# Optimization experiments

Hardware: AMD Instinct MI355X
Metric: run time of the kernel (lower is better)

## Reference

```python
import jax, jax.numpy as jnp
import numpy as np

L, D, H, DH, S, B, V = 8, 1024, 16, 64, 1024, 4, 32000
EPS = 1e-5


def layernorm(x, s, b):
    m = x.mean(-1, keepdims=True)
    v = ((x - m) ** 2).mean(-1, keepdims=True)
    return (x - m) * jax.lax.rsqrt(v + EPS) * s + b


def setup_inputs() -> dict:
    key = jax.random.key(0)
    ks = jax.random.split(key, 12)
    sd = 0.02
    inp = {
        'idx': jax.random.randint(ks[0], (B, S), 0, V),
        'tok_emb': jax.random.normal(ks[1], (V, D), jnp.float32) * sd,
        'pos_emb': jax.random.normal(ks[2], (S, D), jnp.float32) * sd,
        'ln1_s': jnp.ones((L, D), jnp.float32),
        'ln1_b': jnp.zeros((L, D), jnp.float32),
        'wq': jax.random.normal(ks[3], (L, H, D, DH), jnp.float32) * sd,
        'wk': jax.random.normal(ks[4], (L, H, D, DH), jnp.float32) * sd,
        'wv': jax.random.normal(ks[5], (L, H, D, DH), jnp.float32) * sd,
        'wproj': jax.random.normal(ks[6], (L, D, D), jnp.float32) * sd,  # stored [D_in, D_out]
        'ln2_s': jnp.ones((L, D), jnp.float32),
        'ln2_b': jnp.zeros((L, D), jnp.float32),
        'w1': jax.random.normal(ks[7], (L, D, 4 * D), jnp.float32) * sd,
        'b1': jnp.zeros((L, 4 * D), jnp.float32),
        'w2': jax.random.normal(ks[8], (L, 4 * D, D), jnp.float32) * sd,
        'b2': jnp.zeros((L, D), jnp.float32),
        'lnf_s': jnp.ones((D,), jnp.float32),
        'lnf_b': jnp.zeros((D,), jnp.float32),
        'lm_w': jax.random.normal(ks[9], (D, V), jnp.float32) * sd,  # stored [D_in, V]
        'lm_b': jnp.zeros((V,), jnp.float32),
    }
    return inp


def reference(idx, tok_emb, pos_emb, ln1_s, ln1_b, wq, wk, wv, wproj,
              ln2_s, ln2_b, w1, b1, w2, b2, lnf_s, lnf_b, lm_w, lm_b):
    T = idx.shape[1]
    x = tok_emb[idx] + pos_emb[:T]  # [B,T,D]
    mask = jnp.tril(jnp.ones((T, T), bool))
    scale = DH ** -0.5
    for l in range(L):  # fixed small layer count
        h = layernorm(x, ln1_s[l], ln1_b[l])
        q = jnp.einsum('bsd,hde->bhse', h, wq[l])
        k = jnp.einsum('bsd,hde->bhse', h, wk[l])
        v = jnp.einsum('bsd,hde->bhse', h, wv[l])
        att = jnp.einsum('bhse,bhte->bhst', q, k) * scale
        att = jnp.where(mask, att, -jnp.inf)
        att = jax.nn.softmax(att, axis=-1)  # dropout=0.0 -> identity
        o = jnp.einsum('bhst,bhte->bhse', att, v)
        o = o.transpose(0, 2, 1, 3).reshape(x.shape)  # concat heads: [B,T,H*DH]
        x = x + o @ wproj[l]
        h2 = layernorm(x, ln2_s[l], ln2_b[l])
        x = x + jax.nn.relu(h2 @ w1[l] + b1[l]) @ w2[l] + b2[l]
    x = layernorm(x, lnf_s, lnf_b)
    logits = x @ lm_w + lm_b  # [B,T,V]
    return logits
```

## Files before the change

### kernel.cpp

```cpp
#include <hip/hip_runtime.h>
#include <hip/hip_bf16.h>

#define LL 8
#define DD 1024
#define HH 16
#define DHH 64
#define SS 1024
#define BB 4
#define VV 32000
#define MM (BB * SS)

typedef unsigned short u16;
typedef __attribute__((ext_vector_type(8))) short short8v;
typedef __attribute__((ext_vector_type(4))) float f32x4;
typedef unsigned int __attribute__((address_space(1))) guint;
typedef unsigned int __attribute__((address_space(3))) luint;

__device__ __forceinline__ float bf2f_lo(unsigned u) { return __uint_as_float(u << 16); }
__device__ __forceinline__ u16 f2bf(float f) {
  unsigned x = __float_as_uint(f);
  return (u16)((x + 0x7fffu + ((x >> 16) & 1u)) >> 16);
}

__global__ __launch_bounds__(256) void embed_kernel(
    const int* __restrict__ idx, const float* __restrict__ tok,
    const float* __restrict__ pos, float* __restrict__ x) {
  int i = blockIdx.x * blockDim.x + threadIdx.x;
  int elem = i * 4;
  int row = elem / DD;
  int d = elem % DD;
  int s = row % SS;
  int t = idx[row];
  float4 tv = *(const float4*)(tok + (size_t)t * DD + d);
  float4 pv = *(const float4*)(pos + (size_t)s * DD + d);
  tv.x += pv.x; tv.y += pv.y; tv.z += pv.z; tv.w += pv.w;
  *(float4*)(x + (size_t)elem) = tv;
}

__global__ __launch_bounds__(256) void ln_bf16_kernel(
    const float* __restrict__ x, const float* __restrict__ sc,
    const float* __restrict__ bi, u16* __restrict__ out) {
  const int row = blockIdx.x;
  const int tid = threadIdx.x;
  __shared__ float red[4];
  float4 v = ((const float4*)(x + (size_t)row * DD))[tid];
  float s = v.x + v.y + v.z + v.w;
  #pragma unroll
  for (int off = 32; off; off >>= 1) s += __shfl_down(s, off);
  if ((tid & 63) == 0) red[tid >> 6] = s;
  __syncthreads();
  float mean = (red[0] + red[1] + red[2] + red[3]) * (1.f / DD);
  float dx = v.x - mean, dy = v.y - mean, dz = v.z - mean, dw = v.w - mean;
  float vs = dx * dx + dy * dy + dz * dz + dw * dw;
  __syncthreads();
  #pragma unroll
  for (int off = 32; off; off >>= 1) vs += __shfl_down(vs, off);
  if ((tid & 63) == 0) red[tid >> 6] = vs;
  __syncthreads();
  float var = (red[0] + red[1] + red[2] + red[3]) * (1.f / DD);
  float rstd = rsqrtf(var + 1e-5f);
  float4 s4 = ((const float4*)sc)[tid];
  float4 b4 = ((const float4*)bi)[tid];
  ushort4 o;
  o.x = f2bf(dx * rstd * s4.x + b4.x);
  o.y = f2bf(dy * rstd * s4.y + b4.y);
  o.z = f2bf(dz * rstd * s4.z + b4.z);
  o.w = f2bf(dw * rstd * s4.w + b4.w);
  *(ushort4*)(out + (size_t)row * DD + tid * 4) = o;
}

template <bool HEADW>
__global__ __launch_bounds__(256) void convT_kernel(
    const float* __restrict__ W, u16* __restrict__ BT, int K, int N,
    size_t lstride) {
  __shared__ float tile[32][33];
  const int n0 = blockIdx.x * 32, k0 = blockIdx.y * 32, l = blockIdx.z;
  const int tx = threadIdx.x & 31, ty = threadIdx.x >> 5;
  const float* Wl;
  int ld;
  if (HEADW) {
    const int h = n0 >> 6;
    Wl = W + ((size_t)(l * HH + h) * K) * 64 + (n0 & 63);
    ld = 64;
  } else {
    Wl = W + (size_t)l * K * N + n0;
    ld = N;
  }
  #pragma unroll
  for (int i = 0; i < 4; ++i)
    tile[ty + 8 * i][tx] = Wl[(size_t)(k0 + ty + 8 * i) * ld + tx];
  __syncthreads();
  u16* out = BT + (size_t)l * lstride;
  #pragma unroll
  for (int i = 0; i < 4; ++i)
    out[(size_t)(n0 + ty + 8 * i) * K + k0 + tx] = f2bf(tile[tx][ty + 8 * i]);
}

template <bool BIAS, bool RELU, bool RESID, bool OBF16>
__global__ __launch_bounds__(256) void gemm_mfma(
    const u16* __restrict__ A, const u16* __restrict__ BT,
    const float* __restrict__ bias, const float* __restrict__ resid,
    void* __restrict__ Cv, int M, int N, int K) {
  __shared__ u16 As[128 * 64];
  __shared__ u16 Bs[128 * 64];
  const int tid = threadIdx.x;
  const int lane = tid & 63, wave = tid >> 6;
  const int m0 = blockIdx.x * 128, n0 = blockIdx.y * 128;
  const int wr = (wave >> 1) * 64, wc = (wave & 1) * 64;
  const int srow = tid >> 3;
  const int scol = (((tid & 7) ^ (srow & 7)) * 8);
  const u16* Ag = A + (size_t)(m0 + srow) * K + scol;
  const u16* Bg = BT + (size_t)(n0 + srow) * K + scol;

  f32x4 acc[4][4] = {};
  for (int k0 = 0; k0 < K; k0 += 64) {
    #pragma unroll
    for (int c = 0; c < 4; ++c) {
      __builtin_amdgcn_global_load_lds(
          (const guint*)(Ag + k0 + (size_t)c * 32 * K),
          (luint*)(As + c * 2048 + tid * 8), 16, 0, 0);
      __builtin_amdgcn_global_load_lds(
          (const guint*)(Bg + k0 + (size_t)c * 32 * K),
          (luint*)(Bs + c * 2048 + tid * 8), 16, 0, 0);
    }
    __syncthreads();
    #pragma unroll
    for (int kk = 0; kk < 64; kk += 32) {
      const int chA = (((kk >> 3) | (lane >> 4)) ^ (lane & 7)) * 8;
      short8v av[4], bv[4];
      #pragma unroll
      for (int i = 0; i < 4; ++i)
        av[i] = *(const short8v*)(As + (wr + i * 16 + (lane & 15)) * 64 + chA);
      #pragma unroll
      for (int j = 0; j < 4; ++j)
        bv[j] = *(const short8v*)(Bs + (wc + j * 16 + (lane & 15)) * 64 + chA);
      #pragma unroll
      for (int i = 0; i < 4; ++i)
        #pragma unroll
        for (int j = 0; j < 4; ++j)
          acc[i][j] = __builtin_amdgcn_mfma_f32_16x16x32_bf16(av[i], bv[j], acc[i][j], 0, 0, 0);
    }
    __syncthreads();
  }
  #pragma unroll
  for (int i = 0; i < 4; ++i) {
    #pragma unroll
    for (int j = 0; j < 4; ++j) {
      const int col = n0 + wc + j * 16 + (lane & 15);
      #pragma unroll
      for (int r = 0; r < 4; ++r) {
        const int row = m0 + wr + i * 16 + (lane >> 4) * 4 + r;
        float v = acc[i][j][r];
        if (BIAS) v += bias[col];
        if (RELU) v = fmaxf(v, 0.f);
        if (RESID) v += resid[(size_t)row * N + col];
        if (OBF16)
          ((u16*)Cv)[(size_t)row * N + col] = f2bf(v);
        else
          ((float*)Cv)[(size_t)row * N + col] = v;
      }
    }
  }
}

#define LDA_(BUF, KH, F) \
  (*(const short8v*)&As[BUF][KH][(wm * 128 + (F) * 16 + (lane & 15)) * 32 + rg])
#define LDB_(BUF, KH, NF) \
  (*(const short8v*)&Bs[BUF][KH][(wn * 64 + (NF) * 16 + (lane & 15)) * 32 + rg])
#define PH_A(BUF, KH, FB) { a0 = LDA_(BUF, KH, (FB) + 0); a1 = LDA_(BUF, KH, (FB) + 1); \
                            a2 = LDA_(BUF, KH, (FB) + 2); a3 = LDA_(BUF, KH, (FB) + 3); }
#define PH_B(BUF, KH)     { b0 = LDB_(BUF, KH, 0); b1 = LDB_(BUF, KH, 1); \
                            b2 = LDB_(BUF, KH, 2); b3 = LDB_(BUF, KH, 3); }
#define STAGE_A(BUF, KH, KT) do { \
  __builtin_amdgcn_global_load_lds((const guint*)(Abase + (KT) * 64 + (KH) * 32), \
      (luint*)(&As[BUF][KH][tid * 8]), 16, 0, 0); \
  __builtin_amdgcn_global_load_lds((const guint*)(Abase + (size_t)128 * K + (KT) * 64 + (KH) * 32), \
      (luint*)(&As[BUF][KH][(tid + 512) * 8]), 16, 0, 0); \
} while (0)
#define STAGE_B(BUF, KH, KT) do { \
  __builtin_amdgcn_global_load_lds((const guint*)(Bbase + (KT) * 64 + (KH) * 32), \
      (luint*)(&Bs[BUF][KH][tid * 8]), 16, 0, 0); \
  __builtin_amdgcn_global_load_lds((const guint*)(Bbase + (size_t)128 * K + (KT) * 64 + (KH) * 32), \
      (luint*)(&Bs[BUF][KH][(tid + 512) * 8]), 16, 0, 0); \
} while (0)
#define MFMA_ROW(F, AQ) \
  acc[F][0] = __builtin_amdgcn_mfma_f32_16x16x32_bf16(AQ, b0, acc[F][0], 0, 0, 0); \
  acc[F][1] = __builtin_amdgcn_mfma_f32_16x16x32_bf16(AQ, b1, acc[F][1], 0, 0, 0); \
  acc[F][2] = __builtin_amdgcn_mfma_f32_16x16x32_bf16(AQ, b2, acc[F][2], 0, 0, 0); \
  acc[F][3] = __builtin_amdgcn_mfma_f32_16x16x32_bf16(AQ, b3, acc[F][3], 0, 0, 0);
#define MFMA16(FB) MFMA_ROW((FB) + 0, a0) MFMA_ROW((FB) + 1, a1) \
                   MFMA_ROW((FB) + 2, a2) MFMA_ROW((FB) + 3, a3)
#define BARRIER __builtin_amdgcn_s_barrier()
#define LGKM0 asm volatile("s_waitcnt lgkmcnt(0)" ::: "memory")
#define MEMFENCE asm volatile("" ::: "memory")

#define TILE8(CUR, KT, ST1, ST2, V1STR, DOV3, V3STR) { \
  const int cur_ = (CUR); \
  MEMFENCE; \
  PH_B(cur_, 0); PH_A(cur_, 0, 0); \
  if (ST1) { STAGE_A(cur_ ^ 1, 1, (KT) + 1); } \
  BARRIER; LGKM0; \
  __builtin_amdgcn_s_setprio(1); MFMA16(0); __builtin_amdgcn_s_setprio(0); \
  BARRIER; MEMFENCE; \
  PH_A(cur_, 0, 4); \
  if (ST1) { STAGE_B(cur_ ^ 1, 1, (KT) + 1); } \
  asm volatile("s_waitcnt " V1STR ::: "memory"); \
  BARRIER; LGKM0; \
  __builtin_amdgcn_s_setprio(1); MFMA16(4); __builtin_amdgcn_s_setprio(0); \
  BARRIER; MEMFENCE; \
  PH_B(cur_, 1); PH_A(cur_, 1, 0); \
  if (ST2) { STAGE_A(cur_, 0, (KT) + 2); } \
  BARRIER; LGKM0; \
  __builtin_amdgcn_s_setprio(1); MFMA16(0); __builtin_amdgcn_s_setprio(0); \
  BARRIER; MEMFENCE; \
  PH_A(cur_, 1, 4); \
  if (ST2) { STAGE_B(cur_, 0, (KT) + 2); } \
  if (DOV3) { asm volatile("s_waitcnt " V3STR ::: "memory"); } \
  BARRIER; LGKM0; \
  __builtin_amdgcn_s_setprio(1); MFMA16(4); __builtin_amdgcn_s_setprio(0); \
  BARRIER; \
}

template <bool BIAS, bool RELU, bool RESID, bool OBF16>
__global__ __launch_bounds__(512, 2) void gemm8(
    const u16* __restrict__ A, const u16* __restrict__ BT,
    const float* __restrict__ bias, const float* __restrict__ resid,
    void* __restrict__ Cv, int M, int N, int K) {
  __shared__ u16 As[2][2][8192];
  __shared__ u16 Bs[2][2][8192];
  const int tid = threadIdx.x;
  const int lane = tid & 63, wave = tid >> 6;
  const int wm = wave >> 2, wn = wave & 3;
  const int nwg = gridDim.x;
  const int bid = blockIdx.x;
  const int wg = ((nwg & 7) == 0) ? ((bid & 7) * (nwg >> 3) + (bid >> 3)) : bid;
  const int nmt = M >> 8;
  const int m0 = (wg % nmt) * 256;
  const int n0 = (wg / nmt) * 256;
  const int NT = K >> 6;
  const int sr = tid >> 2;
  const int ssc = (((tid & 3) ^ ((tid >> 3) & 3)) * 8);
  const u16* Abase = A + (size_t)(m0 + sr) * K + ssc;
  const u16* Bbase = BT + (size_t)(n0 + sr) * K + ssc;
  const int rg = (((lane >> 4) ^ ((lane >> 1) & 3)) * 8);

  f32x4 acc[8][4] = {};
  short8v a0, a1, a2, a3, b0, b1, b2, b3;

  STAGE_A(0, 0, 0); STAGE_B(0, 0, 0);
  STAGE_A(0, 1, 0); STAGE_B(0, 1, 0);
  STAGE_A(1, 0, 1); STAGE_B(1, 0, 1);
  asm volatile("s_waitcnt vmcnt(8)" ::: "memory");
  BARRIER;

  int kt = 0;
  for (; kt < NT - 2; ++kt) {
    TILE8(kt & 1, kt, true, true, "vmcnt(8)", true, "vmcnt(8)");
  }
  TILE8(kt & 1, kt, true, false, "vmcnt(8)", true, "vmcnt(4)");
  ++kt;
  TILE8(kt & 1, kt, false, false, "vmcnt(0)", false, "vmcnt(0)");

  #pragma unroll
  for (int f = 0; f < 8; ++f) {
    #pragma unroll
    for (int n = 0; n < 4; ++n) {
      const int col = n0 + wn * 64 + n * 16 + (lane & 15);
      #pragma unroll
      for (int r = 0; r < 4; ++r) {
        const int row = m0 + wm * 128 + f * 16 + (lane >> 4) * 4 + r;
        float v = acc[f][n][r];
        if (BIAS) v += bias[col];
        if (RELU) v = fmaxf(v, 0.f);
        if (RESID) v += resid[(size_t)row * N + col];
        if (OBF16)
          ((u16*)Cv)[(size_t)row * N + col] = f2bf(v);
        else
          ((float*)Cv)[(size_t)row * N + col] = v;
      }
    }
  }
}

__global__ __launch_bounds__(256) void gemm_fb(
    const u16* __restrict__ A, const float* __restrict__ B,
    const float* __restrict__ bias, float* __restrict__ C, int M, int N, int K) {
  __shared__ alignas(16) float Asm[16][68];
  __shared__ alignas(16) float Bsm[16][68];
  const int tid = threadIdx.x;
  const int tx = tid & 15, ty = tid >> 4;
  const int m0 = blockIdx.y * 64, n0 = blockIdx.x * 64;
  const int ar = tid >> 2, ac = (tid & 3) * 4;
  const int br = tid >> 4, bc = (tid & 15) * 4;
  float acc[4][4] = {};
  for (int k0 = 0; k0 < K; k0 += 16) {
    ushort4 au = *(const ushort4*)(A + (size_t)(m0 + ar) * K + k0 + ac);
    float4 bv = *(const float4*)(B + (size_t)(k0 + br) * N + n0 + bc);
    Asm[ac + 0][ar] = bf2f_lo(au.x);
    Asm[ac + 1][ar] = bf2f_lo(au.y);
    Asm[ac + 2][ar] = bf2f_lo(au.z);
    Asm[ac + 3][ar] = bf2f_lo(au.w);
    *(float4*)&Bsm[br][bc] = bv;
    __syncthreads();
    #pragma unroll
    for (int kk = 0; kk < 16; ++kk) {
      float4 a = *(const float4*)&Asm[kk][ty * 4];
      float4 b = *(const float4*)&Bsm[kk][tx * 4];
      acc[0][0] += a.x * b.x; acc[0][1] += a.x * b.y; acc[0][2] += a.x * b.z; acc[0][3] += a.x * b.w;
      acc[1][0] += a.y * b.x; acc[1][1] += a.y * b.y; acc[1][2] += a.y * b.z; acc[1][3] += a.y * b.w;
      acc[2][0] += a.z * b.x; acc[2][1] += a.z * b.y; acc[2][2] += a.z * b.z; acc[2][3] += a.z * b.w;
      acc[3][0] += a.w * b.x; acc[3][1] += a.w * b.y; acc[3][2] += a.w * b.z; acc[3][3] += a.w * b.w;
    }
    __syncthreads();
  }
  #pragma unroll
  for (int i = 0; i < 4; ++i) {
    const int m = m0 + ty * 4 + i;
    #pragma unroll
    for (int j = 0; j < 4; ++j) {
      const int n = n0 + tx * 4 + j;
      C[(size_t)m * N + n] = acc[i][j] + bias[n];
    }
  }
}

__global__ __launch_bounds__(256) void attn_mfma(
    const u16* __restrict__ qk, const u16* __restrict__ vt,
    u16* __restrict__ o) {
  __shared__ alignas(16) u16 Ksh[64 * 64];
  __shared__ alignas(16) u16 Vsh[64 * 64];
  __shared__ unsigned Plds[4][16 * 41];
  __shared__ float bcast[4][16];
  const int tid = threadIdx.x;
  const int lane = tid & 63, wave = tid >> 6;
  const int g = lane >> 4, qi = lane & 15;
  const int qt = blockIdx.x, h = blockIdx.y, b = blockIdx.z;
  const int q0w = qt * 64 + wave * 16;
  const int qloc = wave * 16 + qi;

  short8v qf0, qf1;
  {
    const u16* qp = qk + ((size_t)b * SS + q0w + qi) * 2048 + h * DHH + g * 8;
    qf0 = *(const short8v*)qp;
    qf1 = *(const short8v*)(qp + 32);
  }

  f32x4 oacc[4] = {};
  float mrow = -1e30f, lrow = 0.f;

  for (int kt = 0; kt <= qt; ++kt) {
    __syncthreads();
    #pragma unroll
    for (int u = 0; u < 2; ++u) {
      const int unit = tid + 256 * u;
      const int row = unit >> 3, ch = unit & 7;
      const int sch = ch ^ (row & 7);
      __builtin_amdgcn_global_load_lds(
          (const guint*)(qk + ((size_t)b * SS + kt * 64 + row) * 2048 + 1024 + h * DHH + sch * 8),
          (luint*)(Ksh + unit * 8), 16, 0, 0);
      __builtin_amdgcn_global_load_lds(
          (const guint*)(vt + ((size_t)(h * DHH + row)) * MM + b * SS + kt * 64 + sch * 8),
          (luint*)(Vsh + unit * 8), 16, 0, 0);
    }
    __syncthreads();

    f32x4 st[4] = {};
    #pragma unroll
    for (int t = 0; t < 4; ++t) {
      const int row = t * 16 + qi;
      const int swz = (row & 7) << 4;
      short8v kf0 = *(const short8v*)(Ksh + row * 64 + (((g * 16) ^ swz) >> 1));
      short8v kf1 = *(const short8v*)(Ksh + row * 64 + (((64 + g * 16) ^ swz) >> 1));
      st[t] = __builtin_amdgcn_mfma_f32_16x16x32_bf16(kf0, qf0, st[t], 0, 0, 0);
      st[t] = __builtin_amdgcn_mfma_f32_16x16x32_bf16(kf1, qf1, st[t], 0, 0, 0);
    }

    if (kt == qt) {
      #pragma unroll
      for (int t = 0; t < 4; ++t)
        #pragma unroll
        for (int r = 0; r < 4; ++r)
          if (t * 16 + 4 * g + r > qloc) st[t][r] = -1e30f;
    }

    float mt = st[0][0];
    #pragma unroll
    for (int t = 0; t < 4; ++t)
      #pragma unroll
      for (int r = 0; r < 4; ++r) mt = fmaxf(mt, st[t][r]);
    mt = fmaxf(mt, __shfl_xor(mt, 16));
    mt = fmaxf(mt, __shfl_xor(mt, 32));
    const float mnew = fmaxf(mrow, mt * 0.125f);
    const float corr = __expf(mrow - mnew);
    float pl = 0.f;
    #pragma unroll
    for (int t = 0; t < 4; ++t) {
      #pragma unroll
      for (int r2 = 0; r2 < 2; ++r2) {
        float plo = __expf(fmaf(st[t][2 * r2], 0.125f, -mnew));
        float phi = __expf(fmaf(st[t][2 * r2 + 1], 0.125f, -mnew));
        pl += plo + phi;
        Plds[wave][qi * 41 + 8 * t + 2 * g + r2] =
            (unsigned)f2bf(plo) | ((unsigned)f2bf(phi) << 16);
      }
    }
    pl += __shfl_xor(pl, 16);
    pl += __shfl_xor(pl, 32);
    lrow = lrow * corr + pl;
    mrow = mnew;

    if (g == 0) bcast[wave][qi] = corr;
    float c0 = bcast[wave][g * 4 + 0];
    float c1 = bcast[wave][g * 4 + 1];
    float c2 = bcast[wave][g * 4 + 2];
    float c3 = bcast[wave][g * 4 + 3];
    #pragma unroll
    for (int dvt = 0; dvt < 4; ++dvt) {
      oacc[dvt][0] *= c0; oacc[dvt][1] *= c1;
      oacc[dvt][2] *= c2; oacc[dvt][3] *= c3;
    }

    union U8 { unsigned u[4]; short8v s8; };
    U8 pa0, pa1;
    #pragma unroll
    for (int c = 0; c < 4; ++c) {
      pa0.u[c] = Plds[wave][qi * 41 + g * 4 + c];
      pa1.u[c] = Plds[wave][qi * 41 + 16 + g * 4 + c];
    }
    #pragma unroll
    for (int dvt = 0; dvt < 4; ++dvt) {
      const int row = dvt * 16 + qi;
      const int swz = (row & 7) << 4;
      short8v v0 = *(const short8v*)(Vsh + row * 64 + (((g * 16) ^ swz) >> 1));
      short8v v1 = *(const short8v*)(Vsh + row * 64 + (((64 + g * 16) ^ swz) >> 1));
      oacc[dvt] = __builtin_amdgcn_mfma_f32_16x16x32_bf16(pa0.s8, v0, oacc[dvt], 0, 0, 0);
      oacc[dvt] = __builtin_amdgcn_mfma_f32_16x16x32_bf16(pa1.s8, v1, oacc[dvt], 0, 0, 0);
    }
  }

  if (g == 0) bcast[wave][qi] = 1.f / lrow;
  float i0 = bcast[wave][g * 4 + 0];
  float i1 = bcast[wave][g * 4 + 1];
  float i2 = bcast[wave][g * 4 + 2];
  float i3 = bcast[wave][g * 4 + 3];
  #pragma unroll
  for (int dvt = 0; dvt < 4; ++dvt) {
    const int col = h * DHH + dvt * 16 + qi;
    o[((size_t)b * SS + q0w + g * 4 + 0) * DD + col] = f2bf(oacc[dvt][0] * i0);
    o[((size_t)b * SS + q0w + g * 4 + 1) * DD + col] = f2bf(oacc[dvt][1] * i1);
    o[((size_t)b * SS + q0w + g * 4 + 2) * DD + col] = f2bf(oacc[dvt][2] * i2);
    o[((size_t)b * SS + q0w + g * 4 + 3) * DD + col] = f2bf(oacc[dvt][3] * i3);
  }
}

extern "C" void kernel_launch(void* const* d_in, const int* in_sizes, int n_in,
                              void* d_out, int out_size, void* d_ws, size_t ws_size,
                              hipStream_t stream) {
  const int* idx = (const int*)d_in[0];
  const float* tok_emb = (const float*)d_in[1];
  const float* pos_emb = (const float*)d_in[2];
  const float* ln1_s = (const float*)d_in[3];
  const float* ln1_b = (const float*)d_in[4];
  const float* wq = (const float*)d_in[5];
  const float* wk = (const float*)d_in[6];
  const float* wv = (const float*)d_in[7];
  const float* wproj = (const float*)d_in[8];
  const float* ln2_s = (const float*)d_in[9];
  const float* ln2_b = (const float*)d_in[10];
  const float* w1 = (const float*)d_in[11];
  const float* b1 = (const float*)d_in[12];
  const float* w2 = (const float*)d_in[13];
  const float* b2 = (const float*)d_in[14];
  const float* lnf_s = (const float*)d_in[15];
  const float* lnf_b = (const float*)d_in[16];
  const float* lm_w = (const float*)d_in[17];
  const float* lm_b = (const float*)d_in[18];

  const size_t MD = (size_t)MM * DD;

  u16* sc0 = (u16*)d_out;
  u16* BTqk = sc0;
  u16* BTv = BTqk + (size_t)LL * 2048 * DD;
  u16* BTp = BTv + (size_t)LL * DD * DD;
  u16* BTw1 = BTp + (size_t)LL * DD * DD;
  u16* BTw2 = BTw1 + (size_t)LL * DD * 4 * DD;
  u16* qkb = BTw2 + (size_t)LL * DD * 4 * DD;
  u16* vtb = qkb + (size_t)MM * 2048;
  u16* ob = vtb + MD;
  u16* tmp = ob + MD;

  float* x = (float*)d_ws;
  u16* h = (u16*)((char*)d_ws + MD * 4);
  u16* BTlm = (u16*)((char*)d_ws + MD * 4 + MD * 2);
  const bool big_ws = ws_size >= (MD * 4 + MD * 2 + (size_t)VV * DD * 2);

  const dim3 blk(256);

  convT_kernel<true><<<dim3(DD / 32, DD / 32, LL), blk, 0, stream>>>(
      wq, BTqk, DD, DD, (size_t)2048 * DD);
  convT_kernel<true><<<dim3(DD / 32, DD / 32, LL), blk, 0, stream>>>(
      wk, BTqk + (size_t)DD * DD, DD, DD, (size_t)2048 * DD);
  convT_kernel<true><<<dim3(DD / 32, DD / 32, LL), blk, 0, stream>>>(
      wv, BTv, DD, DD, (size_t)DD * DD);
  convT_kernel<false><<<dim3(DD / 32, DD / 32, LL), blk, 0, stream>>>(
      wproj, BTp, DD, DD, (size_t)DD * DD);
  convT_kernel<false><<<dim3(4 * DD / 32, DD / 32, LL), blk, 0, stream>>>(
      w1, BTw1, DD, 4 * DD, (size_t)DD * 4 * DD);
  convT_kernel<false><<<dim3(DD / 32, 4 * DD / 32, LL), blk, 0, stream>>>(
      w2, BTw2, 4 * DD, DD, (size_t)4 * DD * DD);
  if (big_ws)
    convT_kernel<false><<<dim3(VV / 32, DD / 32, 1), blk, 0, stream>>>(
        lm_w, BTlm, DD, VV, (size_t)VV * DD);

  embed_kernel<<<(MM * DD / 4 + 255) / 256, blk, 0, stream>>>(idx, tok_emb, pos_emb, x);

  for (int l = 0; l < LL; ++l) {
    ln_bf16_kernel<<<MM, blk, 0, stream>>>(x, ln1_s + l * DD, ln1_b + l * DD, h);
    gemm8<false, false, false, true><<<dim3((MM / 256) * (2048 / 256)), dim3(512), 0, stream>>>(
        h, BTqk + (size_t)l * 2048 * DD, nullptr, nullptr, qkb, MM, 2048, DD);
    gemm_mfma<false, false, false, true><<<dim3(DD / 128, MM / 128), blk, 0, stream>>>(
        BTv + (size_t)l * DD * DD, h, nullptr, nullptr, vtb, DD, MM, DD);
    attn_mfma<<<dim3(SS / 64, HH, BB), blk, 0, stream>>>(qkb, vtb, ob);
    gemm_mfma<false, false, true, false><<<dim3(MM / 128, DD / 128), blk, 0, stream>>>(
        ob, BTp + (size_t)l * DD * DD, nullptr, x, x, MM, DD, DD);
    ln_bf16_kernel<<<MM, blk, 0, stream>>>(x, ln2_s + l * DD, ln2_b + l * DD, h);
    gemm8<true, true, false, true><<<dim3((MM / 256) * (4 * DD / 256)), dim3(512), 0, stream>>>(
        h, BTw1 + (size_t)l * DD * 4 * DD, b1 + (size_t)l * 4 * DD, nullptr, tmp,
        MM, 4 * DD, DD);
    gemm_mfma<true, false, true, false><<<dim3(MM / 128, DD / 128), blk, 0, stream>>>(
        tmp, BTw2 + (size_t)l * 4 * DD * DD, b2 + (size_t)l * DD, x, x, MM, DD, 4 * DD);
  }

  ln_bf16_kernel<<<MM, blk, 0, stream>>>(x, lnf_s, lnf_b, h);
  if (big_ws) {
    gemm8<true, false, false, false><<<dim3((MM / 256) * (VV / 256)), dim3(512), 0, stream>>>(
        h, BTlm, lm_b, nullptr, (float*)d_out, MM, VV, DD);
  } else {
    gemm_fb<<<dim3(VV / 64, MM / 64), blk, 0, stream>>>(
        h, lm_w, lm_b, (float*)d_out, MM, VV, DD);
  }
}
```

Measured before the change: 2.888 ms.

## Software-pipeline LDS fragment loads with double-buffered registers in GEMM main loop

```diff
diff --git a/kernel.cpp b/kernel.cpp
--- a/kernel.cpp
+++ b/kernel.cpp
@@ -167,10 +167,12 @@
   (*(const short8v*)&As[BUF][KH][(wm * 128 + (F) * 16 + (lane & 15)) * 32 + rg])
 #define LDB_(BUF, KH, NF) \
   (*(const short8v*)&Bs[BUF][KH][(wn * 64 + (NF) * 16 + (lane & 15)) * 32 + rg])
-#define PH_A(BUF, KH, FB) { a0 = LDA_(BUF, KH, (FB) + 0); a1 = LDA_(BUF, KH, (FB) + 1); \
-                            a2 = LDA_(BUF, KH, (FB) + 2); a3 = LDA_(BUF, KH, (FB) + 3); }
-#define PH_B(BUF, KH)     { b0 = LDB_(BUF, KH, 0); b1 = LDB_(BUF, KH, 1); \
-                            b2 = LDB_(BUF, KH, 2); b3 = LDB_(BUF, KH, 3); }
+#define LDS_A(S0,S1,S2,S3, BUF, KH, FB) { \
+  S0 = LDA_(BUF, KH, (FB) + 0); S1 = LDA_(BUF, KH, (FB) + 1); \
+  S2 = LDA_(BUF, KH, (FB) + 2); S3 = LDA_(BUF, KH, (FB) + 3); }
+#define LDS_B(S0,S1,S2,S3, BUF, KH) { \
+  S0 = LDB_(BUF, KH, 0); S1 = LDB_(BUF, KH, 1); \
+  S2 = LDB_(BUF, KH, 2); S3 = LDB_(BUF, KH, 3); }
 #define STAGE_A(BUF, KH, KT) do { \
   __builtin_amdgcn_global_load_lds((const guint*)(Abase + (KT) * 64 + (KH) * 32), \
       (luint*)(&As[BUF][KH][tid * 8]), 16, 0, 0); \
@@ -183,42 +185,59 @@
   __builtin_amdgcn_global_load_lds((const guint*)(Bbase + (size_t)128 * K + (KT) * 64 + (KH) * 32), \
       (luint*)(&Bs[BUF][KH][(tid + 512) * 8]), 16, 0, 0); \
 } while (0)
-#define MFMA_ROW(F, AQ) \
-  acc[F][0] = __builtin_amdgcn_mfma_f32_16x16x32_bf16(AQ, b0, acc[F][0], 0, 0, 0); \
-  acc[F][1] = __builtin_amdgcn_mfma_f32_16x16x32_bf16(AQ, b1, acc[F][1], 0, 0, 0); \
-  acc[F][2] = __builtin_amdgcn_mfma_f32_16x16x32_bf16(AQ, b2, acc[F][2], 0, 0, 0); \
-  acc[F][3] = __builtin_amdgcn_mfma_f32_16x16x32_bf16(AQ, b3, acc[F][3], 0, 0, 0);
-#define MFMA16(FB) MFMA_ROW((FB) + 0, a0) MFMA_ROW((FB) + 1, a1) \
-                   MFMA_ROW((FB) + 2, a2) MFMA_ROW((FB) + 3, a3)
+#define MROW(F, AQ, B0,B1,B2,B3) \
+  acc[F][0] = __builtin_amdgcn_mfma_f32_16x16x32_bf16(AQ, B0, acc[F][0], 0, 0, 0); \
+  acc[F][1] = __builtin_amdgcn_mfma_f32_16x16x32_bf16(AQ, B1, acc[F][1], 0, 0, 0); \
+  acc[F][2] = __builtin_amdgcn_mfma_f32_16x16x32_bf16(AQ, B2, acc[F][2], 0, 0, 0); \
+  acc[F][3] = __builtin_amdgcn_mfma_f32_16x16x32_bf16(AQ, B3, acc[F][3], 0, 0, 0);
+#define MFMA16S(FB, A0,A1,A2,A3, B0,B1,B2,B3) \
+  MROW((FB) + 0, A0, B0,B1,B2,B3) MROW((FB) + 1, A1, B0,B1,B2,B3) \
+  MROW((FB) + 2, A2, B0,B1,B2,B3) MROW((FB) + 3, A3, B0,B1,B2,B3)
 #define BARRIER __builtin_amdgcn_s_barrier()
-#define LGKM0 asm volatile("s_waitcnt lgkmcnt(0)" ::: "memory")
 #define MEMFENCE asm volatile("" ::: "memory")
 
-#define TILE8(CUR, KT, ST1, ST2, V1STR, DOV3, V3STR) { \
+#define TILE4(CUR, KT, ST1, ST2, V1STR, V3STR, LD4, LGK4STR) { \
   const int cur_ = (CUR); \
+   \
   MEMFENCE; \
-  PH_B(cur_, 0); PH_A(cur_, 0, 0); \
+  LDS_A(aN0,aN1,aN2,aN3, cur_, 0, 4); \
   if (ST1) { STAGE_A(cur_ ^ 1, 1, (KT) + 1); } \
-  BARRIER; LGKM0; \
-  __builtin_amdgcn_s_setprio(1); MFMA16(0); __builtin_amdgcn_s_setprio(0); \
-  BARRIER; MEMFENCE; \
-  PH_A(cur_, 0, 4); \
+  asm volatile("s_waitcnt " V1STR ::: "memory"); \
+  asm volatile("s_waitcnt lgkmcnt(4)" ::: "memory"); \
+  BARRIER; \
+  __builtin_amdgcn_s_setprio(1); \
+  MFMA16S(0, aP0,aP1,aP2,aP3, bP0,bP1,bP2,bP3); \
+  __builtin_amdgcn_s_setprio(0); \
+   \
+  MEMFENCE; \
+  LDS_A(aP0,aP1,aP2,aP3, cur_, 1, 0); \
+  LDS_B(bN0,bN1,bN2,bN3, cur_, 1); \
   if (ST1) { STAGE_B(cur_ ^ 1, 1, (KT) + 1); } \
-  asm volatile("s_waitcnt " V1STR ::: "memory"); \
-  BARRIER; LGKM0; \
-  __builtin_amdgcn_s_setprio(1); MFMA16(4); __builtin_amdgcn_s_setprio(0); \
-  BARRIER; MEMFENCE; \
-  PH_B(cur_, 1); PH_A(cur_, 1, 0); \
+  asm volatile("s_waitcnt lgkmcnt(8)" ::: "memory"); \
+  BARRIER; \
+  __builtin_amdgcn_s_setprio(1); \
+  MFMA16S(4, aN0,aN1,aN2,aN3, bP0,bP1,bP2,bP3); \
+  __builtin_amdgcn_s_setprio(0); \
+   \
+  MEMFENCE; \
+  LDS_A(aN0,aN1,aN2,aN3, cur_, 1, 4); \
   if (ST2) { STAGE_A(cur_, 0, (KT) + 2); } \
-  BARRIER; LGKM0; \
-  __builtin_amdgcn_s_setprio(1); MFMA16(0); __builtin_amdgcn_s_setprio(0); \
-  BARRIER; MEMFENCE; \
-  PH_A(cur_, 1, 4); \
+  asm volatile("s_waitcnt " V3STR ::: "memory"); \
+  asm volatile("s_waitcnt lgkmcnt(4)" ::: "memory"); \
+  BARRIER; \
+  __builtin_amdgcn_s_setprio(1); \
+  MFMA16S(0, aP0,aP1,aP2,aP3, bN0,bN1,bN2,bN3); \
+  __builtin_amdgcn_s_setprio(0); \
+   \
+  MEMFENCE; \
+  if (LD4) { LDS_A(aP0,aP1,aP2,aP3, cur_ ^ 1, 0, 0); \
+             LDS_B(bP0,bP1,bP2,bP3, cur_ ^ 1, 0); } \
   if (ST2) { STAGE_B(cur_, 0, (KT) + 2); } \
-  if (DOV3) { asm volatile("s_waitcnt " V3STR ::: "memory"); } \
-  BARRIER; LGKM0; \
-  __builtin_amdgcn_s_setprio(1); MFMA16(4); __builtin_amdgcn_s_setprio(0); \
+  asm volatile("s_waitcnt " LGK4STR ::: "memory"); \
   BARRIER; \
+  __builtin_amdgcn_s_setprio(1); \
+  MFMA16S(4, aN0,aN1,aN2,aN3, bN0,bN1,bN2,bN3); \
+  __builtin_amdgcn_s_setprio(0); \
 }
 
 template <bool BIAS, bool RELU, bool RESID, bool OBF16>
@@ -245,21 +264,25 @@
   const int rg = (((lane >> 4) ^ ((lane >> 1) & 3)) * 8);
 
   f32x4 acc[8][4] = {};
-  short8v a0, a1, a2, a3, b0, b1, b2, b3;
+  short8v aP0, aP1, aP2, aP3, aN0, aN1, aN2, aN3;
+  short8v bP0, bP1, bP2, bP3, bN0, bN1, bN2, bN3;
 
   STAGE_A(0, 0, 0); STAGE_B(0, 0, 0);
   STAGE_A(0, 1, 0); STAGE_B(0, 1, 0);
   STAGE_A(1, 0, 1); STAGE_B(1, 0, 1);
   asm volatile("s_waitcnt vmcnt(8)" ::: "memory");
   BARRIER;
+  MEMFENCE;
+  LDS_A(aP0,aP1,aP2,aP3, 0, 0, 0);
+  LDS_B(bP0,bP1,bP2,bP3, 0, 0);
 
   int kt = 0;
   for (; kt < NT - 2; ++kt) {
-    TILE8(kt & 1, kt, true, true, "vmcnt(8)", true, "vmcnt(8)");
-  }
-  TILE8(kt & 1, kt, true, false, "vmcnt(8)", true, "vmcnt(4)");
+    TILE4(kt & 1, kt, true, true, "vmcnt(6)", "vmcnt(6)", true, "lgkmcnt(8)");
+  }
+  TILE4(kt & 1, kt, true, false, "vmcnt(6)", "vmcnt(4)", true, "lgkmcnt(8)");
   ++kt;
-  TILE8(kt & 1, kt, false, false, "vmcnt(0)", false, "vmcnt(0)");
+  TILE4(kt & 1, kt, false, false, "vmcnt(0)", "vmcnt(0)", false, "lgkmcnt(0)");
 
   #pragma unroll
   for (int f = 0; f < 8; ++f) {
```

New measurement: 2.714 ms. 1.06x faster.
